# Optimization experiments

Measured on AMD Instinct MI355X. Metric: run time of the kernel, lower is better.

## Reference

```python
import jax, jax.numpy as jnp
import numpy as np


def setup_inputs() -> dict:
    key = jax.random.key(0)
    k1, k2 = jax.random.split(key)
    N, D, R = 1_000_000, 128, 50_000
    feat = jax.random.normal(k1, (N, D), dtype=jnp.float32)
    row_ids = jax.random.randint(k2, (N,), 0, R, dtype=jnp.int32)
    return {"feat": feat, "row_ids": row_ids, "num_rows": R}


def reference(feat, row_ids, num_rows):
    # unsorted_segment_max over ragged row groups: [R, D]
    segment_max = jax.ops.segment_max(feat, row_ids, num_segments=num_rows)
    # gather segment max back to node level: [N, D]
    feat_max = segment_max[row_ids]
    feat_residual = feat_max - feat
    # stack residual with original along new axis 1 -> [N, 2, D]
    out = jnp.stack([feat_residual, feat], axis=1)
    return jnp.squeeze(out)
```

## Files before the change

### kernel.cpp

```cpp
#include <hip/hip_runtime.h>
#include <math.h>


#define R_ROWS 50000
#define D_DIM  128
#define CAP    96
#define KREG   16
#define WIN    8

typedef float f32x4 __attribute__((ext_vector_type(4)));


__global__ void __launch_bounds__(256)
zero_u32(unsigned int* __restrict__ p, int n) {
    int i = blockIdx.x * blockDim.x + threadIdx.x;
    int stride = gridDim.x * blockDim.x;
    for (; i < n; i += stride) p[i] = 0u;
}

__global__ void __launch_bounds__(256)
bucket(const int* __restrict__ ids, unsigned int* __restrict__ cnt,
       int* __restrict__ perm, int N) {
    int i = blockIdx.x * blockDim.x + threadIdx.x;
    if (i >= N) return;
    int r = ids[i];
    unsigned int slot = atomicAdd(&cnt[r], 1u);
    if (slot < CAP) perm[r * CAP + slot] = i;
}

__global__ void __launch_bounds__(256)
reduce_emit(const float* __restrict__ feat,
            const int* __restrict__ perm,
            const unsigned int* __restrict__ cnt,
            float* __restrict__ out) {
    int r = blockIdx.x * 4 + (threadIdx.x >> 6);
    if (r >= R_ROWS) return;
    unsigned int c = cnt[r];
    if (!c) return;
    if (c > CAP) c = CAP;
    int lane = threadIdx.x & 63;
    int half = lane >> 5;
    int col4 = lane & 31;
    long long start = (long long)r * CAP;

    f32x4 vv[KREG];
    int   nn[KREG];
    f32x4 m = {-INFINITY, -INFINITY, -INFINITY, -INFINITY};

    #pragma unroll
    for (int j = 0; j < KREG; ++j) {
        unsigned int kk = (unsigned)(2 * j + half);
        nn[j] = (kk < c) ? perm[start + kk] : -1;
    }
    #pragma unroll
    for (int j = 0; j < KREG; ++j) {
        if (nn[j] >= 0) {
            vv[j] = *reinterpret_cast<const f32x4*>(
                feat + (long long)nn[j] * D_DIM + (col4 << 2));
        }
    }
    #pragma unroll
    for (int j = 0; j < KREG; ++j) {
        if (nn[j] >= 0) {
            f32x4 v = vv[j];
            m.x = fmaxf(m.x, v.x); m.y = fmaxf(m.y, v.y);
            m.z = fmaxf(m.z, v.z); m.w = fmaxf(m.w, v.w);
        }
    }
    for (unsigned int w = 2 * KREG; w < c; w += 2 * WIN) {
        int nj[WIN];
        #pragma unroll
        for (int j = 0; j < WIN; ++j) {
            unsigned int kk = w + 2 * j + half;
            nj[j] = (kk < c) ? perm[start + kk] : -1;
        }
        #pragma unroll
        for (int j = 0; j < WIN; ++j) {
            if (nj[j] >= 0) {
                f32x4 v = *reinterpret_cast<const f32x4*>(
                    feat + (long long)nj[j] * D_DIM + (col4 << 2));
                m.x = fmaxf(m.x, v.x); m.y = fmaxf(m.y, v.y);
                m.z = fmaxf(m.z, v.z); m.w = fmaxf(m.w, v.w);
            }
        }
    }

    m.x = fmaxf(m.x, __shfl_xor(m.x, 32));
    m.y = fmaxf(m.y, __shfl_xor(m.y, 32));
    m.z = fmaxf(m.z, __shfl_xor(m.z, 32));
    m.w = fmaxf(m.w, __shfl_xor(m.w, 32));

    #pragma unroll
    for (int j = 0; j < KREG; ++j) {
        if (nn[j] >= 0) {
            f32x4 v = vv[j];
            f32x4 res = m - v;
            f32x4* o = reinterpret_cast<f32x4*>(
                out + (long long)nn[j] * 2 * D_DIM);
            __builtin_nontemporal_store(res, o + col4);
            __builtin_nontemporal_store(v,   o + 32 + col4);
        }
    }
    for (unsigned int w = 2 * KREG; w < c; w += 2 * WIN) {
        int nj[WIN];
        f32x4 vj[WIN];
        #pragma unroll
        for (int j = 0; j < WIN; ++j) {
            unsigned int kk = w + 2 * j + half;
            nj[j] = (kk < c) ? perm[start + kk] : -1;
        }
        #pragma unroll
        for (int j = 0; j < WIN; ++j) {
            if (nj[j] >= 0) {
                vj[j] = *reinterpret_cast<const f32x4*>(
                    feat + (long long)nj[j] * D_DIM + (col4 << 2));
            }
        }
        #pragma unroll
        for (int j = 0; j < WIN; ++j) {
            if (nj[j] >= 0) {
                f32x4 v = vj[j];
                f32x4 res = m - v;
                f32x4* o = reinterpret_cast<f32x4*>(
                    out + (long long)nj[j] * 2 * D_DIM);
                __builtin_nontemporal_store(res, o + col4);
                __builtin_nontemporal_store(v,   o + 32 + col4);
            }
        }
    }
}

extern "C" void kernel_launch(void* const* d_in, const int* in_sizes, int n_in,
                              void* d_out, int out_size, void* d_ws, size_t ws_size,
                              hipStream_t stream) {
    const float* feat = (const float*)d_in[0];
    const int*   ids  = (const int*)d_in[1];
    const int N = in_sizes[0] / D_DIM;

    char* ws = (char*)d_ws;
    unsigned int* cnt  = (unsigned int*)(ws + 0);
    int*          perm = (int*)(ws + 262144);

    const int block = 256;

    zero_u32<<<128, block, 0, stream>>>(cnt, R_ROWS);
    bucket<<<(N + block - 1) / block, block, 0, stream>>>(ids, cnt, perm, N);
    reduce_emit<<<(R_ROWS + 3) / 4, block, 0, stream>>>(
        feat, perm, cnt, (float*)d_out);
}
```

Before: 390.9 us.

## Map full wave per node with float2 columns and vectorize bucket id loads

The reduce kernel now has each 64-lane wave cover one full 128-wide feature row using float2 per lane, instead of two half-waves each covering a row with float4. This removes the cross-half shuffle reduction and doubles the number of register-cached rows (KREG 32) so more nodes avoid a second gather from feat. The bucket kernel reads row ids as int4 with a grid-stride loop, cutting load instructions and launching a fixed 1024 blocks. In exchange it issues narrower 8-byte memory accesses, uses more registers for the cached rows, assumes N is divisible by 4, and drops the row bounds check.

```diff
diff --git a/kernel.cpp b/kernel.cpp
--- a/kernel.cpp
+++ b/kernel.cpp
@@ -5,10 +5,10 @@
 #define R_ROWS 50000
 #define D_DIM  128
 #define CAP    96
-#define KREG   16
+#define KREG   32
 #define WIN    8
 
-typedef float f32x4 __attribute__((ext_vector_type(4)));
+typedef float f32x2 __attribute__((ext_vector_type(2)));
 
 
 __global__ void __launch_bounds__(256)
@@ -19,13 +19,22 @@
 }
 
 __global__ void __launch_bounds__(256)
-bucket(const int* __restrict__ ids, unsigned int* __restrict__ cnt,
-       int* __restrict__ perm, int N) {
+bucket(const int4* __restrict__ ids4, unsigned int* __restrict__ cnt,
+       int* __restrict__ perm, int N4) {
     int i = blockIdx.x * blockDim.x + threadIdx.x;
-    if (i >= N) return;
-    int r = ids[i];
-    unsigned int slot = atomicAdd(&cnt[r], 1u);
-    if (slot < CAP) perm[r * CAP + slot] = i;
+    int stride = gridDim.x * blockDim.x;
+    for (; i < N4; i += stride) {
+        int4 v = ids4[i];
+        int n0 = i * 4;
+        unsigned int s0 = atomicAdd(&cnt[v.x], 1u);
+        if (s0 < CAP) perm[v.x * CAP + s0] = n0;
+        unsigned int s1 = atomicAdd(&cnt[v.y], 1u);
+        if (s1 < CAP) perm[v.y * CAP + s1] = n0 + 1;
+        unsigned int s2 = atomicAdd(&cnt[v.z], 1u);
+        if (s2 < CAP) perm[v.z * CAP + s2] = n0 + 2;
+        unsigned int s3 = atomicAdd(&cnt[v.w], 1u);
+        if (s3 < CAP) perm[v.w * CAP + s3] = n0 + 3;
+    }
 }
 
 __global__ void __launch_bounds__(256)
@@ -33,98 +42,87 @@
             const int* __restrict__ perm,
             const unsigned int* __restrict__ cnt,
             float* __restrict__ out) {
-    int r = blockIdx.x * 4 + (threadIdx.x >> 6);
-    if (r >= R_ROWS) return;
+    int r = __builtin_amdgcn_readfirstlane(blockIdx.x * 4 + (threadIdx.x >> 6));
     unsigned int c = cnt[r];
     if (!c) return;
     if (c > CAP) c = CAP;
     int lane = threadIdx.x & 63;
-    int half = lane >> 5;
-    int col4 = lane & 31;
     long long start = (long long)r * CAP;
+    const f32x2* featp = reinterpret_cast<const f32x2*>(feat);
 
-    f32x4 vv[KREG];
+    f32x2 vv[KREG];
     int   nn[KREG];
-    f32x4 m = {-INFINITY, -INFINITY, -INFINITY, -INFINITY};
+    f32x2 m = {-INFINITY, -INFINITY};
 
     #pragma unroll
     for (int j = 0; j < KREG; ++j) {
-        unsigned int kk = (unsigned)(2 * j + half);
-        nn[j] = (kk < c) ? perm[start + kk] : -1;
+        nn[j] = (j < (int)c) ? perm[start + j] : -1;
     }
     #pragma unroll
     for (int j = 0; j < KREG; ++j) {
         if (nn[j] >= 0) {
-            vv[j] = *reinterpret_cast<const f32x4*>(
-                feat + (long long)nn[j] * D_DIM + (col4 << 2));
+            vv[j] = featp[(long long)nn[j] * (D_DIM / 2) + lane];
         }
     }
     #pragma unroll
     for (int j = 0; j < KREG; ++j) {
         if (nn[j] >= 0) {
-            f32x4 v = vv[j];
-            m.x = fmaxf(m.x, v.x); m.y = fmaxf(m.y, v.y);
-            m.z = fmaxf(m.z, v.z); m.w = fmaxf(m.w, v.w);
+            f32x2 v = vv[j];
+            m.x = fmaxf(m.x, v.x);
+            m.y = fmaxf(m.y, v.y);
         }
     }
-    for (unsigned int w = 2 * KREG; w < c; w += 2 * WIN) {
+    for (unsigned int w = KREG; w < c; w += WIN) {
         int nj[WIN];
         #pragma unroll
         for (int j = 0; j < WIN; ++j) {
-            unsigned int kk = w + 2 * j + half;
+            unsigned int kk = w + j;
             nj[j] = (kk < c) ? perm[start + kk] : -1;
         }
         #pragma unroll
         for (int j = 0; j < WIN; ++j) {
             if (nj[j] >= 0) {
-                f32x4 v = *reinterpret_cast<const f32x4*>(
-                    feat + (long long)nj[j] * D_DIM + (col4 << 2));
-                m.x = fmaxf(m.x, v.x); m.y = fmaxf(m.y, v.y);
-                m.z = fmaxf(m.z, v.z); m.w = fmaxf(m.w, v.w);
+                f32x2 v = featp[(long long)nj[j] * (D_DIM / 2) + lane];
+                m.x = fmaxf(m.x, v.x);
+                m.y = fmaxf(m.y, v.y);
             }
         }
     }
 
-    m.x = fmaxf(m.x, __shfl_xor(m.x, 32));
-    m.y = fmaxf(m.y, __shfl_xor(m.y, 32));
-    m.z = fmaxf(m.z, __shfl_xor(m.z, 32));
-    m.w = fmaxf(m.w, __shfl_xor(m.w, 32));
-
     #pragma unroll
     for (int j = 0; j < KREG; ++j) {
         if (nn[j] >= 0) {
-            f32x4 v = vv[j];
-            f32x4 res = m - v;
-            f32x4* o = reinterpret_cast<f32x4*>(
+            f32x2 v = vv[j];
+            f32x2 res = {m.x - v.x, m.y - v.y};
+            f32x2* o = reinterpret_cast<f32x2*>(
                 out + (long long)nn[j] * 2 * D_DIM);
-            __builtin_nontemporal_store(res, o + col4);
-            __builtin_nontemporal_store(v,   o + 32 + col4);
+            __builtin_nontemporal_store(res, o + lane);
+            __builtin_nontemporal_store(v,   o + (D_DIM / 2) + lane);
         }
     }
-    for (unsigned int w = 2 * KREG; w < c; w += 2 * WIN) {
+    for (unsigned int w = KREG; w < c; w += WIN) {
         int nj[WIN];
-        f32x4 vj[WIN];
+        f32x2 vj[WIN];
         #pragma unroll
         for (int j = 0; j < WIN; ++j) {
-            unsigned int kk = w + 2 * j + half;
+            unsigned int kk = w + j;
             nj[j] = (kk < c) ? perm[start + kk] : -1;
         }
         #pragma unroll
         for (int j = 0; j < WIN; ++j) {
             if (nj[j] >= 0) {
-                vj[j] = *reinterpret_cast<const f32x4*>(
-                    feat + (long long)nj[j] * D_DIM + (col4 << 2));
+                vj[j] = featp[(long long)nj[j] * (D_DIM / 2) + lane];
             }
         }
         #pragma unroll
         for (int j = 0; j < WIN; ++j) {
             if (nj[j] >= 0) {
-                f32x4 v = vj[j];
-                f32x4 res = m - v;
-                f32x4* o = reinterpret_cast<f32x4*>(
+                f32x2 v = vj[j];
+                f32x2 res = {m.x - v.x, m.y - v.y};
+                f32x2* o = reinterpret_cast<f32x2*>(
                     out + (long long)nj[j] * 2 * D_DIM);
-                __builtin_nontemporal_store(res, o + col4);
-                __builtin_nontemporal_store(v,   o + 32 + col4);
+                __builtin_nontemporal_store(res, o + lane);
+                __builtin_nontemporal_store(v,   o + (D_DIM / 2) + lane);
             }
         }
     }
@@ -144,7 +142,8 @@
     const int block = 256;
 
     zero_u32<<<128, block, 0, stream>>>(cnt, R_ROWS);
-    bucket<<<(N + block - 1) / block, block, 0, stream>>>(ids, cnt, perm, N);
-    reduce_emit<<<(R_ROWS + 3) / 4, block, 0, stream>>>(
+    bucket<<<1024, block, 0, stream>>>(
+        (const int4*)ids, cnt, perm, N / 4);
+    reduce_emit<<<R_ROWS / 4, block, 0, stream>>>(
         feat, perm, cnt, (float*)d_out);
 }
```

After: 388.5 us. Within noise of the previous version (-0.6%).
